# Performance work log

Measured on AMD Instinct MI355X. Metric: run time of the kernel, lower is better.

## Reference

```python
import jax, jax.numpy as jnp
import numpy as np

EPS = 1e-5

def setup_inputs() -> dict:
    key = jax.random.key(0)
    ks = jax.random.split(key, 10)
    B, N, D = 1, 20000, 256
    E, H = 320000, 8
    s = 1.0 / np.sqrt(D)
    return {
        "node_embeddings": jax.random.normal(ks[0], (B, N, D), jnp.float32),
        "edge_index": jax.random.randint(ks[1], (2, E), 0, N, jnp.int32),
        "edge_weights": jax.random.uniform(ks[2], (E,), jnp.float32),
        "Wq": jax.random.normal(ks[3], (D, D), jnp.float32) * s,
        "Wk": jax.random.normal(ks[4], (D, D), jnp.float32) * s,
        "Wv": jax.random.normal(ks[5], (D, D), jnp.float32) * s,
        "We": jax.random.normal(ks[6], (H,), jnp.float32),  # edge_encoder weight [num_heads,1] squeezed
        "Wo": jax.random.normal(ks[7], (D, D), jnp.float32) * s,
        "ln_g": jnp.ones((D,), jnp.float32),
        "ln_b": jnp.zeros((D,), jnp.float32),
    }

def reference(node_embeddings, edge_index, edge_weights, Wq, Wk, Wv, We, Wo, ln_g, ln_b):
    B, N, D = node_embeddings.shape
    H = We.shape[0]
    hd = D // H
    scale = 1.0 / np.sqrt(hd)
    residual = node_embeddings

    # projections -> [B, N, H, hd]
    Q = (node_embeddings @ Wq).reshape(B, N, H, hd)
    K = (node_embeddings @ Wk).reshape(B, N, H, hd)
    V = (node_embeddings @ Wv).reshape(B, N, H, hd)

    src = edge_index[0]
    tgt = edge_index[1]
    E = src.shape[0]

    # gather per edge, edge axis leading for segment ops: [E, B, H, hd]
    Q_e = jnp.moveaxis(Q[:, src], 1, 0)
    K_e = jnp.moveaxis(K[:, tgt], 1, 0)
    V_e = jnp.moveaxis(V[:, tgt], 1, 0)

    # per-edge scores [E, B, H]
    scores = (Q_e * K_e).sum(-1) * scale
    bias = edge_weights[:, None] * We[None, :]            # [E, H]
    scores = scores + bias[:, None, :]

    # scatter softmax grouped by source node
    m = jax.ops.segment_max(scores, src, num_segments=N)   # [N, B, H]
    p = jnp.exp(scores - m[src])
    denom = jax.ops.segment_sum(p, src, num_segments=N)    # [N, B, H]
    attn = p / denom[src]                                   # [E, B, H]

    # scatter-add weighted V -> [N, B, H, hd]
    weighted = attn[..., None] * V_e
    agg = jax.ops.segment_sum(weighted.reshape(E, -1), src, num_segments=N)
    agg = agg.reshape(N, B, H, hd)

    attn_out = jnp.moveaxis(agg, 0, 1).reshape(B, N, D)     # [B, N, D]
    out = attn_out @ Wo

    x = out + residual
    mu = x.mean(-1, keepdims=True)
    var = ((x - mu) ** 2).mean(-1, keepdims=True)
    return (x - mu) / jnp.sqrt(var + EPS) * ln_g + ln_b
```

## Files before the change

### kernel.cpp

```cpp
#include <hip/hip_runtime.h>
#include <hip/hip_bf16.h>

typedef __attribute__((ext_vector_type(8))) short short8;
typedef __attribute__((ext_vector_type(4))) int intx4;
typedef __attribute__((ext_vector_type(2))) float floatx2;
typedef __attribute__((ext_vector_type(4))) float f32x4;

#define CH 64

__device__ __forceinline__ ushort f2b(float f) {
  __hip_bfloat16 h = __float2bfloat16(f);
  return *reinterpret_cast<ushort*>(&h);
}
__device__ __forceinline__ float b2f(ushort u) {
  return __uint_as_float(((unsigned)u) << 16);
}
__device__ __forceinline__ unsigned char f2e4(float f) {
  int p = __builtin_amdgcn_cvt_pk_fp8_f32(f, f, 0, false);
  return (unsigned char)(p & 0xff);
}
__device__ __forceinline__ void wave_lds_sync() {
  asm volatile("s_waitcnt lgkmcnt(0)" ::: "memory");
  __builtin_amdgcn_wave_barrier();
}
__device__ __forceinline__ void gload_lds16(const void* g, void* l) {
  __builtin_amdgcn_global_load_lds(
      (const __attribute__((address_space(1))) void*)g,
      (__attribute__((address_space(3))) void*)l, 16, 0, 0);
}

__global__ __launch_bounds__(256) void pre_kernel(
    const float* __restrict__ X, ushort* __restrict__ Xb, int nX,
    const float* __restrict__ Wq, const float* __restrict__ Wk,
    const float* __restrict__ Wv, const float* __restrict__ Wo,
    ushort* __restrict__ Wt, const int* __restrict__ src,
    int* __restrict__ counts, int E, int nxb) {
  __shared__ float L[32][33];
  int b = blockIdx.x;
  int t = threadIdx.x;
  if (b < nxb) {
    int i = (b * 256 + t) * 8;
    if (i >= nX) return;
    float4 x0 = *reinterpret_cast<const float4*>(X + i);
    float4 x1 = *reinterpret_cast<const float4*>(X + i + 4);
    short8 o;
    o[0] = (short)f2b(x0.x); o[1] = (short)f2b(x0.y);
    o[2] = (short)f2b(x0.z); o[3] = (short)f2b(x0.w);
    o[4] = (short)f2b(x1.x); o[5] = (short)f2b(x1.y);
    o[6] = (short)f2b(x1.z); o[7] = (short)f2b(x1.w);
    *reinterpret_cast<short8*>(Xb + i) = o;
  } else if (b < nxb + 256) {
    int bx = b - nxb;
    int mat = bx >> 6;
    int tile = bx & 63;
    int tr = (tile >> 3) * 32;
    int tc = (tile & 7) * 32;
    const float* W = (mat == 0) ? Wq : (mat == 1) ? Wk : (mat == 2) ? Wv : Wo;
    int c = t & 31, r8 = t >> 5;
#pragma unroll
    for (int rr = 0; rr < 4; ++rr) {
      int r = r8 + rr * 8;
      L[r][c] = W[(size_t)(tr + r) * 256 + tc + c];
    }
    __syncthreads();
#pragma unroll
    for (int rr = 0; rr < 4; ++rr) {
      int cc = r8 + rr * 8;
      Wt[(size_t)(mat * 256 + tc + cc) * 256 + tr + c] = f2b(L[c][cc]);
    }
  } else {
    int e = (b - nxb - 256) * 256 + t;
    if (e < E) atomicAdd(&counts[src[e]], 1);
  }
}

__global__ __launch_bounds__(256) void qkv_gemm(
    const ushort* __restrict__ Xb, const ushort* __restrict__ Wt,
    ushort* __restrict__ Qb, unsigned char* __restrict__ Kb8,
    unsigned char* __restrict__ Vb8, int N, int ngemm) {
  __shared__ ushort sA[128 * 64];
  __shared__ ushort sB[128 * 64];
  int bid = blockIdx.x;
  int t = threadIdx.x;
  int q = ngemm >> 3, r = ngemm & 7;
  int xcd = bid & 7;
  int wgid = (xcd < r ? xcd * (q + 1) : r * (q + 1) + (xcd - r) * q) + (bid >> 3);
  int bx = wgid / 6, by = wgid % 6;
  char* cA = (char*)sA;
  char* cB = (char*)sB;
  int lane = t & 63, w = t >> 6;
  int wr = w >> 1, wc = w & 1;
  int row0 = bx * 128;
  int lr = lane & 15, kg = lane >> 4;

  int srow = lane >> 3;
  int skc = (lane & 7) ^ srow;
  int garow[4], gbrow[4];
#pragma unroll
  for (int gi = 0; gi < 4; ++gi) {
    int grp = w * 4 + gi;
    garow[gi] = min(row0 + grp * 8 + srow, N - 1);
    gbrow[gi] = by * 128 + grp * 8 + srow;
  }

  f32x4 acc[4][4] = {};
  for (int k0 = 0; k0 < 256; k0 += 64) {
#pragma unroll
    for (int gi = 0; gi < 4; ++gi) {
      int grp = w * 4 + gi;
      gload_lds16(Xb + (size_t)garow[gi] * 256 + k0 + skc * 8, cA + grp * 1024);
      gload_lds16(Wt + (size_t)gbrow[gi] * 256 + k0 + skc * 8, cB + grp * 1024);
    }
    asm volatile("s_waitcnt vmcnt(0)" ::: "memory");
    __syncthreads();
#pragma unroll
    for (int ks = 0; ks < 2; ++ks) {
      short8 af[4], bf[4];
#pragma unroll
      for (int fr = 0; fr < 4; ++fr) {
        int row = wr * 64 + fr * 16 + lr;
        af[fr] = *reinterpret_cast<const short8*>(
            cA + ((row * 128 + ks * 64 + kg * 16) ^ ((row & 7) << 4)));
      }
#pragma unroll
      for (int fc = 0; fc < 4; ++fc) {
        int col = wc * 64 + fc * 16 + lr;
        bf[fc] = *reinterpret_cast<const short8*>(
            cB + ((col * 128 + ks * 64 + kg * 16) ^ ((col & 7) << 4)));
      }
#pragma unroll
      for (int fr = 0; fr < 4; ++fr)
#pragma unroll
        for (int fc = 0; fc < 4; ++fc)
          acc[fr][fc] = __builtin_amdgcn_mfma_f32_16x16x32_bf16(af[fr], bf[fc], acc[fr][fc], 0, 0, 0);
    }
    __syncthreads();
  }
  int orow = kg * 4;
  int mat = by >> 1;
#pragma unroll
  for (int fr = 0; fr < 4; ++fr)
#pragma unroll
    for (int fc = 0; fc < 4; ++fc)
#pragma unroll
      for (int r2 = 0; r2 < 4; ++r2) {
        int row = row0 + wr * 64 + fr * 16 + orow + r2;
        int col = (by & 1) * 128 + wc * 64 + fc * 16 + lr;
        if (row < N) {
          float v = acc[fr][fc][r2];
          if (mat == 0)      Qb[(size_t)row * 256 + col]  = f2b(v);
          else if (mat == 1) Kb8[(size_t)row * 256 + col] = f2e4(v);
          else               Vb8[(size_t)row * 256 + col] = f2e4(v);
        }
      }
}

__global__ __launch_bounds__(1024) void scan_kernel(
    const int* __restrict__ counts, int* __restrict__ offs, int* __restrict__ cursor, int N) {
  __shared__ int wsum[16];
  __shared__ int wexc[16];
  __shared__ int s_total;
  int t = threadIdx.x;
  int lane = t & 63, wv = t >> 6;
  int per = (N + 1023) >> 10;
  int b0 = t * per;
  int e0 = min(b0 + per, N);
  int sum = 0;
  for (int i = b0; i < e0; ++i) sum += counts[i];
  int x = sum;
#pragma unroll
  for (int off = 1; off < 64; off <<= 1) {
    int y = __shfl_up(x, off);
    if (lane >= off) x += y;
  }
  if (lane == 63) wsum[wv] = x;
  __syncthreads();
  if (t < 64) {
    int s = (lane < 16) ? wsum[lane] : 0;
    int xs = s;
#pragma unroll
    for (int off = 1; off < 16; off <<= 1) {
      int y = __shfl_up(xs, off);
      if (lane >= off) xs += y;
    }
    if (lane < 16) wexc[lane] = xs - s;
    if (lane == 15) s_total = xs;
  }
  __syncthreads();
  int running = wexc[wv] + (x - sum);
  for (int i = b0; i < e0; ++i) {
    int c = counts[i];
    offs[i] = running;
    cursor[i] = running;
    running += c;
  }
  if (t == 0) offs[N] = s_total;
}

__global__ void scatter_kernel(const int* __restrict__ src, const int* __restrict__ tgt,
                               const float* __restrict__ ew, int* __restrict__ cursor,
                               int2* __restrict__ ews, int E) {
  int e = blockIdx.x * blockDim.x + threadIdx.x;
  if (e < E) {
    int pos = atomicAdd(&cursor[src[e]], 1);
    ews[pos] = make_int2(tgt[e], __float_as_int(ew[e]));
  }
}

__global__ __launch_bounds__(256) void attn_kernel(
    const ushort* __restrict__ Qb, const unsigned char* __restrict__ Kb8,
    const unsigned char* __restrict__ Vb8,
    const int* __restrict__ offs, const int2* __restrict__ ews,
    const float* __restrict__ We, ushort* __restrict__ AGGb, int N) {
  __shared__ float s_p[4][CH][8];
  __shared__ int s_tgt[4][CH];
  __shared__ float s_w[4][CH];
  int t = threadIdx.x;
  int w = t >> 6;
  int l = t & 63;
  int i = blockIdx.x * 4 + w;
  if (i >= N) return;
  int e8 = l >> 3;
  int h = l & 7;
  int hacc = l >> 3;
  const float scale = 0.17677669529663687f;
  float we = We[h];

  float qf[32];
  {
    const short8* qr = reinterpret_cast<const short8*>(Qb + (size_t)i * 256 + h * 32);
#pragma unroll
    for (int d = 0; d < 4; ++d) {
      short8 qv = qr[d];
#pragma unroll
      for (int x = 0; x < 8; ++x) qf[d * 8 + x] = b2f((ushort)qv[x]);
    }
  }

  float m = -1e30f, lsum = 0.f;
  float acc0 = 0.f, acc1 = 0.f, acc2 = 0.f, acc3 = 0.f;
  int beg = offs[i], end = offs[i + 1];

  for (int base = beg; base < end; base += CH) {
    int cnt = min(CH, end - base);
    int cnt_pad = (cnt + 7) & ~7;
    {
      bool valid = l < cnt;
      int2 te = valid ? ews[base + l] : make_int2(i, 0);
      s_tgt[w][l] = te.x;
      s_w[w][l] = valid ? __int_as_float(te.y) : 0.f;
    }
    wave_lds_sync();

    float s_local[8];
#pragma unroll
    for (int it = 0; it < 8; ++it) s_local[it] = -1e30f;

    intx4 kc[2], kn[2];
    {
      const intx4* p = reinterpret_cast<const intx4*>(
          Kb8 + (size_t)s_tgt[w][e8] * 256 + h * 32);
      kc[0] = p[0]; kc[1] = p[1];
    }
    if (8 < cnt_pad) {
      const intx4* p = reinterpret_cast<const intx4*>(
          Kb8 + (size_t)s_tgt[w][8 + e8] * 256 + h * 32);
      kn[0] = p[0]; kn[1] = p[1];
    }
    float cmax = -1e30f;
#pragma unroll
    for (int it = 0; it < 8; ++it) {
      if (it * 8 >= cnt_pad) break;
      float dot = 0.f;
#pragma unroll
      for (int c = 0; c < 2; ++c)
#pragma unroll
        for (int e = 0; e < 4; ++e) {
          floatx2 lo = __builtin_amdgcn_cvt_pk_f32_fp8(kc[c][e], false);
          floatx2 hi = __builtin_amdgcn_cvt_pk_f32_fp8(kc[c][e], true);
          int b0 = c * 16 + e * 4;
          dot += qf[b0] * lo[0] + qf[b0 + 1] * lo[1] + qf[b0 + 2] * hi[0] + qf[b0 + 3] * hi[1];
        }
      int j = it * 8 + e8;
      float s = (j < cnt) ? dot * scale + s_w[w][j] * we : -1e30f;
      s_local[it] = s;
      cmax = fmaxf(cmax, s);
      kc[0] = kn[0]; kc[1] = kn[1];
      if ((it + 2) * 8 < cnt_pad) {
        const intx4* p = reinterpret_cast<const intx4*>(
            Kb8 + (size_t)s_tgt[w][(it + 2) * 8 + e8] * 256 + h * 32);
        kn[0] = p[0]; kn[1] = p[1];
      }
    }
    cmax = fmaxf(cmax, __shfl_xor(cmax, 8));
    cmax = fmaxf(cmax, __shfl_xor(cmax, 16));
    cmax = fmaxf(cmax, __shfl_xor(cmax, 32));
    float newm = fmaxf(m, cmax);
    float f = __expf(m - newm);
    float psum = 0.f;
#pragma unroll
    for (int it = 0; it < 8; ++it) {
      if (it * 8 >= cnt_pad) break;
      int j = it * 8 + e8;
      float p = __expf(s_local[it] - newm);
      s_p[w][j][h] = p;
      psum += p;
    }
    psum += __shfl_xor(psum, 8);
    psum += __shfl_xor(psum, 16);
    psum += __shfl_xor(psum, 32);
    lsum = lsum * f + psum;
    m = newm;
    float f_acc = __shfl(f, hacc);
    acc0 *= f_acc; acc1 *= f_acc; acc2 *= f_acc; acc3 *= f_acc;
    wave_lds_sync();

#pragma unroll
    for (int g = 0; g < 8; ++g) {
      if (g * 8 >= cnt_pad) break;
      float pv[8];
      int vv[8];
#pragma unroll
      for (int k = 0; k < 8; ++k) {
        int j = g * 8 + k;
        pv[k] = s_p[w][j][hacc];
        vv[k] = *reinterpret_cast<const int*>(
            Vb8 + (size_t)s_tgt[w][j] * 256 + l * 4);
      }
#pragma unroll
      for (int k = 0; k < 8; ++k) {
        floatx2 lo = __builtin_amdgcn_cvt_pk_f32_fp8(vv[k], false);
        floatx2 hi = __builtin_amdgcn_cvt_pk_f32_fp8(vv[k], true);
        acc0 += pv[k] * lo[0];
        acc1 += pv[k] * lo[1];
        acc2 += pv[k] * hi[0];
        acc3 += pv[k] * hi[1];
      }
    }
    wave_lds_sync();
  }
  float lsum_acc = __shfl(lsum, hacc);
  float rinv = (lsum_acc > 0.f) ? 1.f / lsum_acc : 0.f;
  ushort4 o = make_ushort4(f2b(acc0 * rinv), f2b(acc1 * rinv),
                           f2b(acc2 * rinv), f2b(acc3 * rinv));
  *reinterpret_cast<ushort4*>(AGGb + (size_t)i * 256 + l * 4) = o;
}

__global__ __launch_bounds__(256) void out_ln(
    const ushort* __restrict__ AGGb, const ushort* __restrict__ Wot,
    const float* __restrict__ X, const float* __restrict__ g, const float* __restrict__ bb,
    float* __restrict__ out, int N) {
  __shared__ ushort sA[64 * 64];
  __shared__ ushort sB[256 * 64];
  char* cA = (char*)sA;
  char* cB = (char*)sB;
  int t = threadIdx.x;
  int lane = t & 63, w = t >> 6;
  int row0 = blockIdx.x * 64;
  int lr = lane & 15, kg = lane >> 4;
  f32x4 acc[16] = {};
  for (int k0 = 0; k0 < 256; k0 += 64) {
#pragma unroll
    for (int it = 0; it < 2; ++it) {
      int slot = t + it * 256;
      int row = slot >> 3, kc = slot & 7;
      int grow = min(row0 + row, N - 1);
      short8 va = *reinterpret_cast<const short8*>(AGGb + (size_t)grow * 256 + k0 + kc * 8);
      *reinterpret_cast<short8*>(cA + ((row * 128 + kc * 16) ^ ((row & 7) << 4))) = va;
    }
#pragma unroll
    for (int it = 0; it < 8; ++it) {
      int slot = t + it * 256;
      int col = slot >> 3, kc = slot & 7;
      short8 vb = *reinterpret_cast<const short8*>(Wot + (size_t)col * 256 + k0 + kc * 8);
      *reinterpret_cast<short8*>(cB + ((col * 128 + kc * 16) ^ ((col & 7) << 4))) = vb;
    }
    __syncthreads();
#pragma unroll
    for (int ks = 0; ks < 2; ++ks) {
      int arow = w * 16 + lr;
      short8 a = *reinterpret_cast<const short8*>(
          cA + ((arow * 128 + ks * 64 + kg * 16) ^ ((arow & 7) << 4)));
#pragma unroll
      for (int fc = 0; fc < 16; ++fc) {
        int col = fc * 16 + lr;
        short8 b = *reinterpret_cast<const short8*>(
            cB + ((col * 128 + ks * 64 + kg * 16) ^ ((col & 7) << 4)));
        acc[fc] = __builtin_amdgcn_mfma_f32_16x16x32_bf16(a, b, acc[fc], 0, 0, 0);
      }
    }
    __syncthreads();
  }
  float g16[16], b16[16];
#pragma unroll
  for (int fc = 0; fc < 16; ++fc) {
    g16[fc] = g[fc * 16 + lr];
    b16[fc] = bb[fc * 16 + lr];
  }
#pragma unroll
  for (int r = 0; r < 4; ++r) {
    int rowl = kg * 4 + r;
    int grow = row0 + w * 16 + rowl;
    int growc = min(grow, N - 1);
    float xv[16];
    float s = 0.f, ss = 0.f;
#pragma unroll
    for (int fc = 0; fc < 16; ++fc) {
      float v = acc[fc][r] + X[(size_t)growc * 256 + fc * 16 + lr];
      xv[fc] = v;
      s += v;
      ss += v * v;
    }
    s += __shfl_xor(s, 1);  ss += __shfl_xor(ss, 1);
    s += __shfl_xor(s, 2);  ss += __shfl_xor(ss, 2);
    s += __shfl_xor(s, 4);  ss += __shfl_xor(ss, 4);
    s += __shfl_xor(s, 8);  ss += __shfl_xor(ss, 8);
    float mu = s * (1.f / 256.f);
    float var = ss * (1.f / 256.f) - mu * mu;
    float rs = rsqrtf(var + 1e-5f);
    if (grow < N) {
#pragma unroll
      for (int fc = 0; fc < 16; ++fc)
        out[(size_t)grow * 256 + fc * 16 + lr] = (xv[fc] - mu) * rs * g16[fc] + b16[fc];
    }
  }
}

extern "C" void kernel_launch(void* const* d_in, const int* in_sizes, int n_in,
                              void* d_out, int out_size, void* d_ws, size_t ws_size,
                              hipStream_t stream) {
  const float* X  = (const float*)d_in[0];
  const int* eidx = (const int*)d_in[1];
  const float* ew = (const float*)d_in[2];
  const float* Wq = (const float*)d_in[3];
  const float* Wk = (const float*)d_in[4];
  const float* Wv = (const float*)d_in[5];
  const float* We = (const float*)d_in[6];
  const float* Wo = (const float*)d_in[7];
  const float* g  = (const float*)d_in[8];
  const float* b  = (const float*)d_in[9];
  int N = in_sizes[0] / 256;
  int E = in_sizes[1] / 2;
  const int* src = eidx;
  const int* tgt = eidx + E;
  float* out = (float*)d_out;

  char* w = (char*)d_ws;
  ushort* Xb   = (ushort*)w;        w += (size_t)N * 256 * 2;
  ushort* Wt   = (ushort*)w;        w += (size_t)1024 * 256 * 2;
  ushort* Qb   = (ushort*)w;        w += (size_t)N * 256 * 2;
  unsigned char* Kb8 = (unsigned char*)w;  w += (size_t)N * 256;
  unsigned char* Vb8 = (unsigned char*)w;  w += (size_t)N * 256;
  ushort* AGGb = (ushort*)w;        w += (size_t)N * 256 * 2;
  int* counts  = (int*)w;           w += (size_t)N * 4;
  int* offs    = (int*)w;           w += (size_t)(N + 1) * 4;
  int* cursor  = (int*)w;           w += (size_t)N * 4;
  int2* ews    = (int2*)w;          w += (size_t)E * 8;
  const ushort* Wot = Wt + (size_t)768 * 256;

  hipMemsetAsync(counts, 0, (size_t)N * 4, stream);

  int nX = N * 256;
  int nxb = (nX / 8 + 255) / 256;
  int nhist = (E + 255) / 256;
  pre_kernel<<<nxb + 256 + nhist, 256, 0, stream>>>(X, Xb, nX, Wq, Wk, Wv, Wo, Wt, src, counts, E, nxb);

  int ngemm = ((N + 127) / 128) * 6;
  qkv_gemm<<<ngemm, 256, 0, stream>>>(Xb, Wt, Qb, Kb8, Vb8, N, ngemm);

  scan_kernel<<<1, 1024, 0, stream>>>(counts, offs, cursor, N);
  scatter_kernel<<<(E + 255) / 256, 256, 0, stream>>>(src, tgt, ew, cursor, ews, E);
  attn_kernel<<<(N + 3) / 4, 256, 0, stream>>>(Qb, Kb8, Vb8, offs, ews, We, AGGb, N);
  out_ln<<<(N + 63) / 64, 256, 0, stream>>>(AGGb, Wot, X, g, b, out, N);
}
```

Before: 158.7 us.

## Double-buffer QKV GEMM, move histogram into GEMM launch, packed float2 math in attention

Removes the hipMemsetAsync by zeroing counts inside pre_kernel. The edge histogram atomics move into extra blocks of the qkv_gemm launch so they overlap with the GEMM. The GEMM K loop is double-buffered in LDS so the next tile loads while MFMAs run, at twice the shared memory. The attention kernel uses floatx2 vectors for the QK dot and the V accumulation, aiming at packed FP32 instructions.

After: 146.0 us. -8.0%, faster.

```diff
diff --git a/kernel.cpp b/kernel.cpp
--- a/kernel.cpp
+++ b/kernel.cpp
@@ -33,8 +33,7 @@
     const float* __restrict__ X, ushort* __restrict__ Xb, int nX,
     const float* __restrict__ Wq, const float* __restrict__ Wk,
     const float* __restrict__ Wv, const float* __restrict__ Wo,
-    ushort* __restrict__ Wt, const int* __restrict__ src,
-    int* __restrict__ counts, int E, int nxb) {
+    ushort* __restrict__ Wt, int* __restrict__ counts, int N, int nxb) {
   __shared__ float L[32][33];
   int b = blockIdx.x;
   int t = threadIdx.x;
@@ -69,25 +68,29 @@
       Wt[(size_t)(mat * 256 + tc + cc) * 256 + tr + c] = f2b(L[c][cc]);
     }
   } else {
-    int e = (b - nxb - 256) * 256 + t;
-    if (e < E) atomicAdd(&counts[src[e]], 1);
+    int i = (b - nxb - 256) * 256 + t;
+    if (i < N) counts[i] = 0;
   }
 }
 
 __global__ __launch_bounds__(256) void qkv_gemm(
     const ushort* __restrict__ Xb, const ushort* __restrict__ Wt,
     ushort* __restrict__ Qb, unsigned char* __restrict__ Kb8,
-    unsigned char* __restrict__ Vb8, int N, int ngemm) {
-  __shared__ ushort sA[128 * 64];
-  __shared__ ushort sB[128 * 64];
+    unsigned char* __restrict__ Vb8, const int* __restrict__ src,
+    int* __restrict__ counts, int N, int E, int ngemm) {
+  __shared__ ushort sA[2][8192];
+  __shared__ ushort sB[2][8192];
   int bid = blockIdx.x;
   int t = threadIdx.x;
+  if (bid >= ngemm) {
+    int e = (bid - ngemm) * 256 + t;
+    if (e < E) atomicAdd(&counts[src[e]], 1);
+    return;
+  }
   int q = ngemm >> 3, r = ngemm & 7;
   int xcd = bid & 7;
   int wgid = (xcd < r ? xcd * (q + 1) : r * (q + 1) + (xcd - r) * q) + (bid >> 3);
   int bx = wgid / 6, by = wgid % 6;
-  char* cA = (char*)sA;
-  char* cB = (char*)sB;
   int lane = t & 63, w = t >> 6;
   int wr = w >> 1, wc = w & 1;
   int row0 = bx * 128;
@@ -103,16 +106,27 @@
     gbrow[gi] = by * 128 + grp * 8 + srow;
   }
 
+#define STAGE(BA, BB, K0)                                                       \
+  {                                                                             \
+    _Pragma("unroll") for (int gi = 0; gi < 4; ++gi) {                          \
+      int grp = w * 4 + gi;                                                     \
+      gload_lds16(Xb + (size_t)garow[gi] * 256 + (K0) + skc * 8,                \
+                  (char*)(BA) + grp * 1024);                                    \
+      gload_lds16(Wt + (size_t)gbrow[gi] * 256 + (K0) + skc * 8,                \
+                  (char*)(BB) + grp * 1024);                                    \
+    }                                                                           \
+  }
+
   f32x4 acc[4][4] = {};
-  for (int k0 = 0; k0 < 256; k0 += 64) {
-#pragma unroll
-    for (int gi = 0; gi < 4; ++gi) {
-      int grp = w * 4 + gi;
-      gload_lds16(Xb + (size_t)garow[gi] * 256 + k0 + skc * 8, cA + grp * 1024);
-      gload_lds16(Wt + (size_t)gbrow[gi] * 256 + k0 + skc * 8, cB + grp * 1024);
-    }
-    asm volatile("s_waitcnt vmcnt(0)" ::: "memory");
-    __syncthreads();
+  STAGE(sA[0], sB[0], 0);
+  asm volatile("s_waitcnt vmcnt(0)" ::: "memory");
+  __syncthreads();
+#pragma unroll
+  for (int k = 0; k < 4; ++k) {
+    int cur = k & 1;
+    if (k < 3) STAGE(sA[cur ^ 1], sB[cur ^ 1], (k + 1) * 64);
+    char* cA = (char*)sA[cur];
+    char* cB = (char*)sB[cur];
 #pragma unroll
     for (int ks = 0; ks < 2; ++ks) {
       short8 af[4], bf[4];
@@ -134,8 +148,10 @@
         for (int fc = 0; fc < 4; ++fc)
           acc[fr][fc] = __builtin_amdgcn_mfma_f32_16x16x32_bf16(af[fr], bf[fc], acc[fr][fc], 0, 0, 0);
     }
+    asm volatile("s_waitcnt vmcnt(0)" ::: "memory");
     __syncthreads();
   }
+#undef STAGE
   int orow = kg * 4;
   int mat = by >> 1;
 #pragma unroll
@@ -226,19 +242,25 @@
   const float scale = 0.17677669529663687f;
   float we = We[h];
 
-  float qf[32];
+  floatx2 qf2[16];
   {
     const short8* qr = reinterpret_cast<const short8*>(Qb + (size_t)i * 256 + h * 32);
 #pragma unroll
     for (int d = 0; d < 4; ++d) {
       short8 qv = qr[d];
 #pragma unroll
-      for (int x = 0; x < 8; ++x) qf[d * 8 + x] = b2f((ushort)qv[x]);
+      for (int x = 0; x < 4; ++x) {
+        floatx2 p;
+        p[0] = b2f((ushort)qv[2 * x]);
+        p[1] = b2f((ushort)qv[2 * x + 1]);
+        qf2[d * 4 + x] = p;
+      }
     }
   }
 
   float m = -1e30f, lsum = 0.f;
-  float acc0 = 0.f, acc1 = 0.f, acc2 = 0.f, acc3 = 0.f;
+  floatx2 accA = {0.f, 0.f};
+  floatx2 accB = {0.f, 0.f};
   int beg = offs[i], end = offs[i + 1];
 
   for (int base = beg; base < end; base += CH) {
@@ -271,16 +293,18 @@
 #pragma unroll
     for (int it = 0; it < 8; ++it) {
       if (it * 8 >= cnt_pad) break;
-      float dot = 0.f;
+      floatx2 dot2 = {0.f, 0.f};
 #pragma unroll
       for (int c = 0; c < 2; ++c)
 #pragma unroll
         for (int e = 0; e < 4; ++e) {
           floatx2 lo = __builtin_amdgcn_cvt_pk_f32_fp8(kc[c][e], false);
           floatx2 hi = __builtin_amdgcn_cvt_pk_f32_fp8(kc[c][e], true);
-          int b0 = c * 16 + e * 4;
-          dot += qf[b0] * lo[0] + qf[b0 + 1] * lo[1] + qf[b0 + 2] * hi[0] + qf[b0 + 3] * hi[1];
+          int b0 = c * 8 + e * 2;
+          dot2 += qf2[b0] * lo;
+          dot2 += qf2[b0 + 1] * hi;
         }
+      float dot = dot2[0] + dot2[1];
       int j = it * 8 + e8;
       float s = (j < cnt) ? dot * scale + s_w[w][j] * we : -1e30f;
       s_local[it] = s;
@@ -312,7 +336,9 @@
     lsum = lsum * f + psum;
     m = newm;
     float f_acc = __shfl(f, hacc);
-    acc0 *= f_acc; acc1 *= f_acc; acc2 *= f_acc; acc3 *= f_acc;
+    floatx2 f2v = {f_acc, f_acc};
+    accA *= f2v;
+    accB *= f2v;
     wave_lds_sync();
 
 #pragma unroll
@@ -331,18 +357,17 @@
       for (int k = 0; k < 8; ++k) {
         floatx2 lo = __builtin_amdgcn_cvt_pk_f32_fp8(vv[k], false);
         floatx2 hi = __builtin_amdgcn_cvt_pk_f32_fp8(vv[k], true);
-        acc0 += pv[k] * lo[0];
-        acc1 += pv[k] * lo[1];
-        acc2 += pv[k] * hi[0];
-        acc3 += pv[k] * hi[1];
+        floatx2 p2 = {pv[k], pv[k]};
+        accA += p2 * lo;
+        accB += p2 * hi;
       }
     }
     wave_lds_sync();
   }
   float lsum_acc = __shfl(lsum, hacc);
   float rinv = (lsum_acc > 0.f) ? 1.f / lsum_acc : 0.f;
-  ushort4 o = make_ushort4(f2b(acc0 * rinv), f2b(acc1 * rinv),
-                           f2b(acc2 * rinv), f2b(acc3 * rinv));
+  ushort4 o = make_ushort4(f2b(accA[0] * rinv), f2b(accA[1] * rinv),
+                           f2b(accB[0] * rinv), f2b(accB[1] * rinv));
   *reinterpret_cast<ushort4*>(AGGb + (size_t)i * 256 + l * 4) = o;
 }
 
@@ -458,15 +483,14 @@
   int2* ews    = (int2*)w;          w += (size_t)E * 8;
   const ushort* Wot = Wt + (size_t)768 * 256;
 
-  hipMemsetAsync(counts, 0, (size_t)N * 4, stream);
-
   int nX = N * 256;
   int nxb = (nX / 8 + 255) / 256;
+  int nzero = (N + 255) / 256;
+  pre_kernel<<<nxb + 256 + nzero, 256, 0, stream>>>(X, Xb, nX, Wq, Wk, Wv, Wo, Wt, counts, N, nxb);
+
+  int ngemm = ((N + 127) / 128) * 6;
   int nhist = (E + 255) / 256;
-  pre_kernel<<<nxb + 256 + nhist, 256, 0, stream>>>(X, Xb, nX, Wq, Wk, Wv, Wo, Wt, src, counts, E, nxb);
-
-  int ngemm = ((N + 127) / 128) * 6;
-  qkv_gemm<<<ngemm, 256, 0, stream>>>(Xb, Wt, Qb, Kb8, Vb8, N, ngemm);
+  qkv_gemm<<<ngemm + nhist, 256, 0, stream>>>(Xb, Wt, Qb, Kb8, Vb8, src, counts, N, E, ngemm);
 
   scan_kernel<<<1, 1024, 0, stream>>>(counts, offs, cursor, N);
   scatter_kernel<<<(E + 255) / 256, 256, 0, stream>>>(src, tgt, ew, cursor, ews, E);
```
